# Optimization experiments

Hardware: AMD Instinct MI355X
Metric: run time of the kernel (lower is better)

Reference implementation:

```python
import jax, jax.numpy as jnp
import numpy as np

B, T = 128, 512          # batch, sequence length (padded game length)
F_IN = 19 * 19           # flattened Go board features
H = 128                  # n_hid
P = 19 * 19 + 1          # policy classes: board points + pass


def setup_inputs() -> dict:
    key = jax.random.key(0)
    ks = jax.random.split(key, 8)
    s = 0.05  # init scale
    return {
        "states": jax.random.normal(ks[0], (B, T, F_IN), jnp.float32),
        "moves": jax.random.randint(ks[1], (B, T), 0, P, jnp.int32),
        "values": jax.random.uniform(ks[2], (B, T), jnp.float32, -1.0, 1.0),
        # LSTM layer 0: concat([x, h]) @ W0 + b0, gates [i, f, g, o]
        "W0": jax.random.normal(ks[3], (F_IN + H, 4 * H), jnp.float32) * s,
        "b0": jnp.zeros((4 * H,), jnp.float32),
        # LSTM layer 1
        "W1": jax.random.normal(ks[4], (H + H, 4 * H), jnp.float32) * s,
        "b1": jnp.zeros((4 * H,), jnp.float32),
        # policy head (size**2 + 1 logits), value head (tanh scalar)
        "Wp": jax.random.normal(ks[5], (H, P), jnp.float32) * s,
        "bp": jnp.zeros((P,), jnp.float32),
        "Wv": jax.random.normal(ks[6], (H, 1), jnp.float32) * s,
        "bv": jnp.zeros((1,), jnp.float32),
    }


def _lstm_cell(h, c, x, W, b):
    # TF LSTMCell: z = [x; h] @ W + b, forget bias 1.0
    z = jnp.concatenate([x, h], axis=-1) @ W + b
    i, f, g, o = jnp.split(z, 4, axis=-1)
    c_new = jax.nn.sigmoid(f + 1.0) * c + jax.nn.sigmoid(i) * jnp.tanh(g)
    h_new = jax.nn.sigmoid(o) * jnp.tanh(c_new)
    return h_new, c_new


def reference(states, moves, values, W0, b0, W1, b1, Wp, bp, Wv, bv):
    b = states.shape[0]
    zeros = jnp.zeros((b, H), states.dtype)

    def step(carry, x_t):
        h0, c0, h1, c1 = carry
        h0, c0 = _lstm_cell(h0, c0, x_t, W0, b0)
        h1, c1 = _lstm_cell(h1, c1, h0, W1, b1)
        return (h0, c0, h1, c1), h1

    _, hs = jax.lax.scan(step, (zeros, zeros, zeros, zeros),
                         jnp.swapaxes(states, 0, 1))  # hs: [T, B, H]
    outputs = jnp.swapaxes(hs, 0, 1)                  # [B, T, H]

    policy_logits = outputs @ Wp + bp                 # [B, T, P]
    winners = jnp.tanh(outputs @ Wv + bv)[..., 0]     # [B, T]

    mask = (values != -9.0).astype(jnp.float32)
    n_mask = mask.sum()

    logp = jax.nn.log_softmax(policy_logits, axis=-1)
    xent = -jnp.take_along_axis(logp, moves[..., None].astype(jnp.int32), axis=-1)[..., 0]
    policy_loss = (mask * xent).sum() / n_mask
    value_loss = (mask * jnp.square(winners - values)).sum() / n_mask
    acc = (moves == jnp.argmax(policy_logits, axis=-1).astype(moves.dtype)).astype(jnp.float32).mean()
    return jnp.stack([policy_loss, value_loss, acc])
```

## Files before the change

### kernel.cpp

```cpp
#include <hip/hip_runtime.h>
#include <hip/hip_bf16.h>
#include <stdint.h>


typedef short v8s __attribute__((ext_vector_type(8)));
typedef float v4f __attribute__((ext_vector_type(4)));

#define MFMA_B16(a,b,c) __builtin_amdgcn_mfma_f32_16x16x32_bf16((a),(b),(c),0,0,0)

#define NT     512
#define FIN    361
#define KP0    384
#define NPC    362
#define NPP    368

#define OFF_Z    ((size_t)0)
#define OFF_H0   ((size_t)67108864)
#define OFF_H1   ((size_t)83886080)
#define OFF_W0XT ((size_t)100663296)
#define OFF_WPT  ((size_t)101187584)
#define OFF_B0P  ((size_t)101281792)
#define OFF_BPP  ((size_t)101285888)
#define OFF_ACC  ((size_t)101287936)

static __device__ __forceinline__ short f2b(float f) {
  __hip_bfloat16 h = __float2bfloat16(f);
  union { __hip_bfloat16 h; short s; } cv; cv.h = h; return cv.s;
}
static __device__ __forceinline__ float b2f(unsigned int lo16) {
  union { unsigned u; float f; } cv; cv.u = lo16 << 16; return cv.f;
}

static __device__ __forceinline__ void sync_lds() {
  __builtin_amdgcn_sched_barrier(0);
  asm volatile("s_waitcnt lgkmcnt(0)" ::: "memory");
  __builtin_amdgcn_s_barrier();
  __builtin_amdgcn_sched_barrier(0);
}

__global__ __launch_bounds__(256) void k_conv_weights(
    const float* __restrict__ W0, const float* __restrict__ b0,
    const float* __restrict__ Wp, const float* __restrict__ bp,
    char* __restrict__ ws) {
  int idx = blockIdx.x * 256 + threadIdx.x;
  __hip_bfloat16* W0xT = (__hip_bfloat16*)(ws + OFF_W0XT);
  __hip_bfloat16* WpT  = (__hip_bfloat16*)(ws + OFF_WPT);
  float* b0p = (float*)(ws + OFF_B0P);
  float* bpp = (float*)(ws + OFF_BPP);
  float* acc = (float*)(ws + OFF_ACC);

  if (idx < 196608) {
    int np = idx / 384, k = idx - np * 384;
    int n = (np >> 2) + 128 * (np & 3);
    float v = (k < FIN) ? W0[(size_t)k * 512 + n] : 0.f;
    W0xT[idx] = __float2bfloat16(v);
    return;
  }
  idx -= 196608;
  if (idx < 47104) {
    int p = idx >> 7, k = idx & 127;
    WpT[idx] = __float2bfloat16(p < NPC ? Wp[(size_t)k * NPC + p] : 0.f);
    return;
  }
  idx -= 47104;
  if (idx < 512) {
    int n = (idx >> 2) + 128 * (idx & 3);
    b0p[idx] = b0[n] + (((idx & 3) == 1) ? 1.0f : 0.0f);
    return;
  }
  idx -= 512;
  if (idx < NPP) { bpp[idx] = (idx < NPC) ? bp[idx] : -1e30f; return; }
  idx -= NPP;
  if (idx < 4) { acc[idx] = 0.f; return; }
}

template<int KTOT, bool AF32>
__global__ __launch_bounds__(256) void k_gemm(
    const void* __restrict__ Ap, const __hip_bfloat16* __restrict__ BT,
    const float* __restrict__ bias, __hip_bfloat16* __restrict__ C) {
  __shared__ char sm[65536];
  const int tid = threadIdx.x;
  const int l = tid & 63, wm = tid >> 6;
  const int c = l & 15, lg = l >> 4;
  const int m0 = blockIdx.x * 128;
  const int n0 = blockIdx.y * 128;
  constexpr int NS = KTOT / 64;

  uint4 ra[4], rb[4];
  float fa[32];

  auto LD = [&](int ks) {
#pragma unroll
    for (int i = 0; i < 4; i++) {
      int idx = i * 4096 + tid * 16;
      int row = idx >> 7, colb = idx & 127;
      if constexpr (AF32) {
        int r = m0 + row;
        const float* src = (const float*)Ap + ((size_t)(r & 127) * NT + (r >> 7)) * FIN;
        int kb = ks * 64 + (colb >> 1);
#pragma unroll
        for (int u = 0; u < 8; u++) {
          int kf = kb + u;
          fa[i * 8 + u] = (kf < FIN) ? src[kf] : 0.f;
        }
      } else {
        ra[i] = *(const uint4*)((const char*)Ap + ((size_t)(m0 + row) * KTOT + ks * 64) * 2 + colb);
      }
      rb[i] = *(const uint4*)((const char*)BT + ((size_t)(n0 + row) * KTOT + ks * 64) * 2 + colb);
    }
  };
  auto ST = [&](int bsel) {
#pragma unroll
    for (int i = 0; i < 4; i++) {
      int idx = i * 4096 + tid * 16;
      int row = idx >> 7, colb = idx & 127;
      int sw = colb ^ ((row & 7) << 4);
      if constexpr (AF32) {
        v8s w;
#pragma unroll
        for (int u = 0; u < 8; u++) w[u] = f2b(fa[i * 8 + u]);
        *(v8s*)(sm + bsel * 16384 + row * 128 + sw) = w;
      } else {
        *(uint4*)(sm + bsel * 16384 + row * 128 + sw) = ra[i];
      }
      *(uint4*)(sm + 32768 + bsel * 16384 + row * 128 + sw) = rb[i];
    }
  };

  v4f acc[2][8];
  v4f z4 = {0.f, 0.f, 0.f, 0.f};
#pragma unroll
  for (int mt = 0; mt < 2; mt++)
#pragma unroll
    for (int nt = 0; nt < 8; nt++) acc[mt][nt] = z4;

  LD(0); ST(0);
  __syncthreads();
  for (int ks = 0; ks < NS; ks++) {
    if (ks + 1 < NS) LD(ks + 1);
    const int bsel = ks & 1;
#pragma unroll
    for (int kk = 0; kk < 2; kk++) {
      int bir = kk * 64 + lg * 16;
      v8s af[2];
#pragma unroll
      for (int mt = 0; mt < 2; mt++) {
        int row = wm * 32 + mt * 16 + c;
        af[mt] = *(v8s*)(sm + bsel * 16384 + row * 128 + (bir ^ ((row & 7) << 4)));
      }
#pragma unroll
      for (int nt = 0; nt < 8; nt++) {
        int n = nt * 16 + c;
        v8s bf = *(v8s*)(sm + 32768 + bsel * 16384 + n * 128 + (bir ^ ((n & 7) << 4)));
#pragma unroll
        for (int mt = 0; mt < 2; mt++) acc[mt][nt] = MFMA_B16(af[mt], bf, acc[mt][nt]);
      }
    }
    if (ks + 1 < NS) ST((ks + 1) & 1);
    __syncthreads();
  }

#pragma unroll
  for (int mt = 0; mt < 2; mt++)
#pragma unroll
    for (int nt = 0; nt < 8; nt++) {
      int colp = n0 + nt * 16 + c;
      float bs = bias[colp];
#pragma unroll
      for (int j = 0; j < 4; j++) {
        int row = m0 + wm * 32 + mt * 16 + lg * 4 + j;
        C[(size_t)row * 512 + colp] = __float2bfloat16(acc[mt][nt][j] + bs);
      }
    }
}

__global__ __launch_bounds__(512) void k_scanA(
    const __hip_bfloat16* __restrict__ Z, const float* __restrict__ Wfull,
    int row0, __hip_bfloat16* __restrict__ hout) {
  __shared__ char sm[8192];
  const int tid = threadIdx.x;
  const int l = tid & 63, wv = tid >> 6;
  const int c = l & 15, lg = l >> 4;
  const int b0 = blockIdx.x * 4;
  const int m_ = 16 * wv + c;

  v8s breg[4][4];
#pragma unroll
  for (int g = 0; g < 4; g++) {
    int n = g * 128 + m_;
#pragma unroll
    for (int kk = 0; kk < 4; kk++) {
      v8s w;
#pragma unroll
      for (int i = 0; i < 8; i++)
        w[i] = f2b(Wfull[(size_t)(row0 + kk * 32 + lg * 8 + i) * 512 + n]);
      breg[kk][g] = w;
    }
  }
  for (int e = tid; e < 4096; e += 512) *(short*)(sm + e * 2) = 0;

  float cst = 0.f;
  auto ZLD = [&](int t) -> uint2 {
    return *(const uint2*)(Z + ((size_t)t * 128 + b0 + lg) * 512 + m_ * 4);
  };
  uint2 zA = ZLD(0), zB = ZLD(1), zC;
  __syncthreads();

  v4f z4 = {0.f, 0.f, 0.f, 0.f};
  const int wrow = 4 * lg;
  const int woff = wrow * 256 + ((m_ * 2) ^ ((wrow & 7) << 4));
  for (int t = 0; t < NT; t++) {
    v4f acc[4];
#pragma unroll
    for (int g = 0; g < 4; g++) acc[g] = z4;
    const int hb = (t & 1) * 4096;
#pragma unroll
    for (int kk = 0; kk < 4; kk++) {
      int bir = kk * 64 + lg * 16;
      v8s a = *(v8s*)(sm + hb + c * 256 + (bir ^ ((c & 7) << 4)));
#pragma unroll
      for (int g = 0; g < 4; g++) acc[g] = MFMA_B16(a, breg[kk][g], acc[g]);
    }
    if (t + 2 < NT) zC = ZLD(t + 2);

    float xi = acc[0][0] + b2f(zA.x & 0xffffu);
    float xf = acc[1][0] + b2f(zA.x >> 16);
    float xg = acc[2][0] + b2f(zA.y & 0xffffu);
    float xo = acc[3][0] + b2f(zA.y >> 16);
    float ei = __expf(-xi);
    float ef = __expf(-xf);
    float eg = __expf(2.f * xg);
    float eo = __expf(-xo);
    float cn = cst * __builtin_amdgcn_rcpf(1.f + ef)
             + (eg - 1.f) * __builtin_amdgcn_rcpf((1.f + ei) * (eg + 1.f));
    cst = cn;
    float ec = __expf(2.f * cn);
    float hv = (ec - 1.f) * __builtin_amdgcn_rcpf((1.f + eo) * (ec + 1.f));
    short hbits = f2b(hv);
    *(short*)(sm + ((t + 1) & 1) * 4096 + woff) = hbits;
    union { short s; __hip_bfloat16 h; } cv; cv.s = hbits;
    hout[((size_t)t * 128 + b0 + lg) * 128 + m_] = cv.h;
    zA = zB; zB = zC;
    sync_lds();
  }
}

__global__ __launch_bounds__(512) void k_scanB(
    const unsigned short* __restrict__ H0, const float* __restrict__ W1f,
    const float* __restrict__ b1, __hip_bfloat16* __restrict__ hout) {
  __shared__ char sm[8192];
  const int tid = threadIdx.x;
  const int l = tid & 63, wv = tid >> 6;
  const int c = l & 15, lg = l >> 4;
  const int b0 = blockIdx.x * 4;
  const int m_ = 16 * wv + c;

  v8s bregX[4][4], bregH[4][4];
#pragma unroll
  for (int g = 0; g < 4; g++) {
    int n = g * 128 + m_;
#pragma unroll
    for (int kk = 0; kk < 4; kk++) {
      v8s wx, wh;
#pragma unroll
      for (int i = 0; i < 8; i++) {
        int k = kk * 32 + lg * 8 + i;
        wx[i] = f2b(W1f[(size_t)k * 512 + n]);
        wh[i] = f2b(W1f[(size_t)(128 + k) * 512 + n]);
      }
      bregX[kk][g] = wx; bregH[kk][g] = wh;
    }
  }
  float bq[4];
#pragma unroll
  for (int g = 0; g < 4; g++)
    bq[g] = b1[g * 128 + m_] + ((g == 1) ? 1.0f : 0.0f);
  for (int e = tid; e < 4096; e += 512) *(short*)(sm + e * 2) = 0;

  uint4 u4z = {0u, 0u, 0u, 0u};
  uint4 hqA[4], hqB[4];
#pragma unroll
  for (int kk = 0; kk < 4; kk++) { hqA[kk] = u4z; hqB[kk] = u4z; }
  auto HLD = [&](int t, uint4* dst) {
    if ((c & 3) == 0) {
      const char* p = (const char*)H0 +
          (((size_t)t * 128 + b0 + (c >> 2)) * 128 + lg * 8) * 2;
#pragma unroll
      for (int kk = 0; kk < 4; kk++) dst[kk] = *(const uint4*)(p + kk * 64);
    }
  };
  HLD(0, hqA);

  float cst = 0.f;
  const int wrow = 4 * lg;
  const int woff = wrow * 256 + ((m_ * 2) ^ ((wrow & 7) << 4));
  __syncthreads();

  auto STEP = [&](int t, uint4* cur, uint4* nxt) {
    if (t + 1 < NT) HLD(t + 1, nxt);
    v4f acc[4];
#pragma unroll
    for (int g = 0; g < 4; g++) acc[g] = (v4f){bq[g], bq[g], bq[g], bq[g]};
    const int hb = (t & 1) * 4096;
#pragma unroll
    for (int kk = 0; kk < 4; kk++) {
      int bir = kk * 64 + lg * 16;
      v8s a = *(v8s*)(sm + hb + c * 256 + (bir ^ ((c & 7) << 4)));
#pragma unroll
      for (int g = 0; g < 4; g++) acc[g] = MFMA_B16(a, bregH[kk][g], acc[g]);
    }
#pragma unroll
    for (int kk = 0; kk < 4; kk++) {
      union { uint4 q; v8s v; } u; u.q = cur[kk];
#pragma unroll
      for (int g = 0; g < 4; g++) acc[g] = MFMA_B16(u.v, bregX[kk][g], acc[g]);
    }
    float xi = acc[0][0];
    float xf = acc[1][0];
    float xg = acc[2][0];
    float xo = acc[3][0];
    float ei = __expf(-xi);
    float ef = __expf(-xf);
    float eg = __expf(2.f * xg);
    float eo = __expf(-xo);
    float cn = cst * __builtin_amdgcn_rcpf(1.f + ef)
             + (eg - 1.f) * __builtin_amdgcn_rcpf((1.f + ei) * (eg + 1.f));
    cst = cn;
    float ec = __expf(2.f * cn);
    float hv = (ec - 1.f) * __builtin_amdgcn_rcpf((1.f + eo) * (ec + 1.f));
    short hbits = f2b(hv);
    *(short*)(sm + ((t + 1) & 1) * 4096 + woff) = hbits;
    union { short s; __hip_bfloat16 h; } cv; cv.s = hbits;
    hout[((size_t)t * 128 + b0 + lg) * 128 + m_] = cv.h;
    sync_lds();
  };

  for (int t = 0; t < NT; t += 2) {
    STEP(t, hqA, hqB);
    STEP(t + 1, hqB, hqA);
  }
}

__global__ __launch_bounds__(256) void k_heads(
    const __hip_bfloat16* __restrict__ Hh, const __hip_bfloat16* __restrict__ WpT,
    const float* __restrict__ bpp, const float* __restrict__ Wv,
    const float* __restrict__ bv, const int* __restrict__ moves,
    const float* __restrict__ values, float* __restrict__ accum) {
  __shared__ char sm[110592];
  const int tid = threadIdx.x;
  const int l = tid & 63, wm = tid >> 6;
  const int c = l & 15, lg = l >> 4;
  const int r0 = blockIdx.x * 64;

#pragma unroll
  for (int i = 0; i < 4; i++) {
    int idx = i * 4096 + tid * 16;
    int row = idx >> 8, colb = idx & 255;
    uint4 v = *(const uint4*)((const char*)Hh + (size_t)r0 * 256 + idx);
    *(uint4*)(sm + row * 256 + (colb ^ ((row & 7) << 4))) = v;
  }
#pragma unroll
  for (int i = 0; i < 23; i++) {
    int idx = i * 4096 + tid * 16;
    int row = idx >> 8, colb = idx & 255;
    uint4 v = *(const uint4*)((const char*)WpT + idx);
    *(uint4*)(sm + 16384 + row * 256 + (colb ^ ((row & 7) << 4))) = v;
  }
  __syncthreads();

  v4f acc[23];
  v4f z4 = {0.f, 0.f, 0.f, 0.f};
#pragma unroll
  for (int q = 0; q < 23; q++) acc[q] = z4;
#pragma unroll
  for (int kk = 0; kk < 4; kk++) {
    int bir = kk * 64 + lg * 16;
    int ar = wm * 16 + c;
    v8s a = *(v8s*)(sm + ar * 256 + (bir ^ ((ar & 7) << 4)));
#pragma unroll
    for (int q = 0; q < 23; q++) {
      int n = q * 16 + c;
      v8s b = *(v8s*)(sm + 16384 + n * 256 + (bir ^ ((n & 7) << 4)));
      acc[q] = MFMA_B16(a, b, acc[q]);
    }
  }
  float bq[23];
#pragma unroll
  for (int q = 0; q < 23; q++) bq[q] = bpp[q * 16 + c];

  float tp = 0.f, tv = 0.f, ta = 0.f, tn = 0.f;
#pragma unroll
  for (int j = 0; j < 4; j++) {
    int rloc = lg * 4 + j;
    int r = r0 + wm * 16 + rloc;
    int t = r >> 7, b = r & 127;
    int mv = moves[(size_t)b * NT + t];
    float val = values[(size_t)b * NT + t];
    float msk = (val != -9.0f) ? 1.f : 0.f;

    float pmax = -3.0e38f;
#pragma unroll
    for (int q = 0; q < 23; q++) pmax = fmaxf(pmax, acc[q][j] + bq[q]);
#pragma unroll
    for (int d = 1; d < 16; d <<= 1) pmax = fmaxf(pmax, __shfl_xor(pmax, d, 64));
    float ps = 0.f;
#pragma unroll
    for (int q = 0; q < 23; q++) ps += __expf((acc[q][j] + bq[q]) - pmax);
#pragma unroll
    for (int d = 1; d < 16; d <<= 1) ps += __shfl_xor(ps, d, 64);
    float lse = pmax + __logf(ps);

    int qm = mv >> 4, cm = mv & 15;
    float mlv = 0.f;
#pragma unroll
    for (int q = 0; q < 23; q++) if (q == qm) mlv = acc[q][j] + bq[q];
    mlv = __shfl(mlv, (l & 48) + cm, 64);
    float xent = lse - mlv;

    float amx = -3.0e38f; int aix = 0;
#pragma unroll
    for (int q = 0; q < 23; q++) {
      float v = acc[q][j] + bq[q];
      if (v > amx) { amx = v; aix = q * 16 + c; }
    }
#pragma unroll
    for (int d = 1; d < 16; d <<= 1) {
      float ov = __shfl_xor(amx, d, 64);
      int oi = __shfl_xor(aix, d, 64);
      if (ov > amx || (ov == amx && oi < aix)) { amx = ov; aix = oi; }
    }

    float pd = 0.f;
    int vrow = wm * 16 + rloc;
#pragma unroll
    for (int i = 0; i < 8; i++) {
      int k = c * 8 + i;
      short hv = *(short*)(sm + vrow * 256 + ((k * 2) ^ ((vrow & 7) << 4)));
      pd += b2f((unsigned short)hv) * Wv[k];
    }
#pragma unroll
    for (int d = 1; d < 16; d <<= 1) pd += __shfl_xor(pd, d, 64);
    float eo = __expf(2.f * (pd + bv[0]));
    float win = (eo - 1.f) * __builtin_amdgcn_rcpf(eo + 1.f);
    float dv = win - val;

    if (c == 0) {
      tp += msk * xent;
      tv += msk * dv * dv;
      ta += (aix == mv) ? 1.f : 0.f;
      tn += msk;
    }
  }
  tp += __shfl_xor(tp, 16, 64); tp += __shfl_xor(tp, 32, 64);
  tv += __shfl_xor(tv, 16, 64); tv += __shfl_xor(tv, 32, 64);
  ta += __shfl_xor(ta, 16, 64); ta += __shfl_xor(ta, 32, 64);
  tn += __shfl_xor(tn, 16, 64); tn += __shfl_xor(tn, 32, 64);
  if (l == 0) {
    atomicAdd(accum + 0, tp);
    atomicAdd(accum + 1, tv);
    atomicAdd(accum + 2, ta);
    atomicAdd(accum + 3, tn);
  }
}

__global__ void k_final(const float* __restrict__ accum, float* __restrict__ out) {
  if (threadIdx.x == 0) {
    float nm = accum[3];
    out[0] = accum[0] / nm;
    out[1] = accum[1] / nm;
    out[2] = accum[2] / 65536.0f;
  }
}

extern "C" void kernel_launch(void* const* d_in, const int* in_sizes, int n_in,
                              void* d_out, int out_size, void* d_ws, size_t ws_size,
                              hipStream_t stream) {
  (void)in_sizes; (void)n_in; (void)out_size; (void)ws_size;
  const float* states = (const float*)d_in[0];
  const int*   moves  = (const int*)d_in[1];
  const float* values = (const float*)d_in[2];
  const float* W0 = (const float*)d_in[3];
  const float* b0 = (const float*)d_in[4];
  const float* W1 = (const float*)d_in[5];
  const float* b1 = (const float*)d_in[6];
  const float* Wp = (const float*)d_in[7];
  const float* bp = (const float*)d_in[8];
  const float* Wv = (const float*)d_in[9];
  const float* bv = (const float*)d_in[10];
  char* ws = (char*)d_ws;

  __hip_bfloat16* zbuf = (__hip_bfloat16*)(ws + OFF_Z);
  __hip_bfloat16* h0   = (__hip_bfloat16*)(ws + OFF_H0);
  unsigned short* h0u  = (unsigned short*)(ws + OFF_H0);
  __hip_bfloat16* h1   = (__hip_bfloat16*)(ws + OFF_H1);
  __hip_bfloat16* W0xT = (__hip_bfloat16*)(ws + OFF_W0XT);
  __hip_bfloat16* WpT  = (__hip_bfloat16*)(ws + OFF_WPT);
  float* b0p = (float*)(ws + OFF_B0P);
  float* bpp = (float*)(ws + OFF_BPP);
  float* acc = (float*)(ws + OFF_ACC);

  k_conv_weights<<<956, 256, 0, stream>>>(W0, b0, Wp, bp, ws);
  k_gemm<KP0, true><<<dim3(512, 4), 256, 0, stream>>>(states, W0xT, b0p, zbuf);
  k_scanA<<<32, 512, 0, stream>>>(zbuf, W0, FIN, h0);
  k_scanB<<<32, 512, 0, stream>>>(h0u, W1, b1, h1);
  k_heads<<<1024, 256, 0, stream>>>(h1, WpT, bpp, Wv, bv, moves, values, acc);
  k_final<<<1, 1, 0, stream>>>(acc, (float*)d_out);
}
```

Measured before the change: 1.002 ms.

## Fuse both LSTM layer scans into one wavefront-specialized kernel with FP8 layer-1 MFMA

Result: slower. 1.034 ms (+3.2%).

```diff
diff --git a/kernel.cpp b/kernel.cpp
--- a/kernel.cpp
+++ b/kernel.cpp
@@ -7,6 +7,7 @@
 typedef float v4f __attribute__((ext_vector_type(4)));
 
 #define MFMA_B16(a,b,c) __builtin_amdgcn_mfma_f32_16x16x32_bf16((a),(b),(c),0,0,0)
+#define MFMA_F8(a,b,c)  __builtin_amdgcn_mfma_f32_16x16x32_fp8_fp8((a),(b),(c),0,0,0)
 
 #define NT     512
 #define FIN    361
@@ -15,7 +16,6 @@
 #define NPP    368
 
 #define OFF_Z    ((size_t)0)
-#define OFF_H0   ((size_t)67108864)
 #define OFF_H1   ((size_t)83886080)
 #define OFF_W0XT ((size_t)100663296)
 #define OFF_WPT  ((size_t)101187584)
@@ -29,6 +29,22 @@
 }
 static __device__ __forceinline__ float b2f(unsigned int lo16) {
   union { unsigned u; float f; } cv; cv.u = lo16 << 16; return cv.f;
+}
+static __device__ __forceinline__ unsigned f2e4m3(float f) {
+  union { float f; unsigned u; } cv; cv.f = f;
+  unsigned s = (cv.u >> 31) << 7;
+  float a = fabsf(f);
+  a = fminf(a, 448.f);
+  unsigned code;
+  if (a >= 0.015625f) {
+    union { float f; unsigned u; } m; m.f = a;
+    unsigned u = m.u + 0x7FFFF + ((m.u >> 20) & 1);
+    code = (u >> 20) - 960;
+    if (code > 126u) code = 126u;
+  } else {
+    code = (unsigned)rintf(a * 512.f);
+  }
+  return s | code;
 }
 
 static __device__ __forceinline__ void sync_lds() {
@@ -174,170 +190,140 @@
     }
 }
 
-__global__ __launch_bounds__(512) void k_scanA(
-    const __hip_bfloat16* __restrict__ Z, const float* __restrict__ Wfull,
-    int row0, __hip_bfloat16* __restrict__ hout) {
-  __shared__ char sm[8192];
+__global__ __launch_bounds__(1024, 4) void k_scan12(
+    const __hip_bfloat16* __restrict__ Z, const float* __restrict__ W0f,
+    const float* __restrict__ W1f, const float* __restrict__ b1,
+    __hip_bfloat16* __restrict__ h1out) {
+  __shared__ char sm[16384];
   const int tid = threadIdx.x;
   const int l = tid & 63, wv = tid >> 6;
   const int c = l & 15, lg = l >> 4;
-  const int b0 = blockIdx.x * 4;
-  const int m_ = 16 * wv + c;
-
-  v8s breg[4][4];
-#pragma unroll
-  for (int g = 0; g < 4; g++) {
-    int n = g * 128 + m_;
-#pragma unroll
-    for (int kk = 0; kk < 4; kk++) {
-      v8s w;
-#pragma unroll
-      for (int i = 0; i < 8; i++)
-        w[i] = f2b(Wfull[(size_t)(row0 + kk * 32 + lg * 8 + i) * 512 + n]);
-      breg[kk][g] = w;
-    }
-  }
-  for (int e = tid; e < 4096; e += 512) *(short*)(sm + e * 2) = 0;
-
-  float cst = 0.f;
-  auto ZLD = [&](int t) -> uint2 {
-    return *(const uint2*)(Z + ((size_t)t * 128 + b0 + lg) * 512 + m_ * 4);
-  };
-  uint2 zA = ZLD(0), zB = ZLD(1), zC;
-  __syncthreads();
-
+  const int role = wv >> 3, rw = wv & 7;
+  const int B0 = blockIdx.x * 4;
+  const int m_ = 16 * rw + c;
+  const int row = 4 * lg;
   v4f z4 = {0.f, 0.f, 0.f, 0.f};
-  const int wrow = 4 * lg;
-  const int woff = wrow * 256 + ((m_ * 2) ^ ((wrow & 7) << 4));
-  for (int t = 0; t < NT; t++) {
-    v4f acc[4];
-#pragma unroll
-    for (int g = 0; g < 4; g++) acc[g] = z4;
-    const int hb = (t & 1) * 4096;
-#pragma unroll
-    for (int kk = 0; kk < 4; kk++) {
-      int bir = kk * 64 + lg * 16;
-      v8s a = *(v8s*)(sm + hb + c * 256 + (bir ^ ((c & 7) << 4)));
-#pragma unroll
-      for (int g = 0; g < 4; g++) acc[g] = MFMA_B16(a, breg[kk][g], acc[g]);
-    }
-    if (t + 2 < NT) zC = ZLD(t + 2);
-
-    float xi = acc[0][0] + b2f(zA.x & 0xffffu);
-    float xf = acc[1][0] + b2f(zA.x >> 16);
-    float xg = acc[2][0] + b2f(zA.y & 0xffffu);
-    float xo = acc[3][0] + b2f(zA.y >> 16);
-    float ei = __expf(-xi);
-    float ef = __expf(-xf);
-    float eg = __expf(2.f * xg);
-    float eo = __expf(-xo);
-    float cn = cst * __builtin_amdgcn_rcpf(1.f + ef)
-             + (eg - 1.f) * __builtin_amdgcn_rcpf((1.f + ei) * (eg + 1.f));
-    cst = cn;
-    float ec = __expf(2.f * cn);
-    float hv = (ec - 1.f) * __builtin_amdgcn_rcpf((1.f + eo) * (ec + 1.f));
-    short hbits = f2b(hv);
-    *(short*)(sm + ((t + 1) & 1) * 4096 + woff) = hbits;
-    union { short s; __hip_bfloat16 h; } cv; cv.s = hbits;
-    hout[((size_t)t * 128 + b0 + lg) * 128 + m_] = cv.h;
-    zA = zB; zB = zC;
+
+  for (int e = tid * 4; e < 16384; e += 1024 * 4) *(int*)(sm + e) = 0;
+
+  if (role == 0) {
+    v8s breg[4][4];
+#pragma unroll
+    for (int kk = 0; kk < 4; kk++)
+#pragma unroll
+      for (int g = 0; g < 4; g++) {
+        int n = g * 128 + m_;
+        v8s w;
+#pragma unroll
+        for (int i = 0; i < 8; i++)
+          w[i] = f2b(W0f[(size_t)(FIN + kk * 32 + lg * 8 + i) * 512 + n]);
+        breg[kk][g] = w;
+      }
+
+    uint2 zA, zB, zC;
+    auto ZLD = [&](int t) -> uint2 {
+      return *(const uint2*)(Z + ((size_t)t * 128 + B0 + lg) * 512 + m_ * 4);
+    };
+    zA = ZLD(0); zB = ZLD(1);
+    float cst = 0.f;
+    const int wb16 = row * 256 + (((m_ >> 3) ^ row) << 4) + ((m_ * 2) & 15);
+    const int wf8  = row * 128 + (((m_ >> 3) ^ row) << 3) + (m_ & 7);
+    __syncthreads();
+
+    for (int s = 0; s < NT; s++) {
+      const int abase = ((s + 1) & 1) * 4096;
+      v4f acc[4];
+#pragma unroll
+      for (int g = 0; g < 4; g++) acc[g] = z4;
+#pragma unroll
+      for (int kk = 0; kk < 4; kk++) {
+        v8s a = *(v8s*)(sm + abase + c * 256 + ((((kk * 4 + lg) ^ c) & 15) << 4));
+#pragma unroll
+        for (int g = 0; g < 4; g++) acc[g] = MFMA_B16(a, breg[kk][g], acc[g]);
+      }
+      if (s + 2 < NT) zC = ZLD(s + 2);
+
+      float xi = acc[0][0] + b2f(zA.x & 0xffffu);
+      float xf = acc[1][0] + b2f(zA.x >> 16);
+      float xg = acc[2][0] + b2f(zA.y & 0xffffu);
+      float xo = acc[3][0] + b2f(zA.y >> 16);
+      float ei = __expf(-xi);
+      float ef = __expf(-xf);
+      float eg = __expf(2.f * xg);
+      float eo = __expf(-xo);
+      float cn = cst * __builtin_amdgcn_rcpf(1.f + ef)
+               + (eg - 1.f) * __builtin_amdgcn_rcpf((1.f + ei) * (eg + 1.f));
+      cst = cn;
+      float ec = __expf(2.f * cn);
+      float hv = (ec - 1.f) * __builtin_amdgcn_rcpf((1.f + eo) * (ec + 1.f));
+      *(short*)(sm + (s & 1) * 4096 + wb16) = f2b(hv);
+      *(unsigned char*)(sm + 8192 + (s & 1) * 2048 + wf8) = (unsigned char)f2e4m3(hv);
+      zA = zB; zB = zC;
+      sync_lds();
+    }
     sync_lds();
-  }
-}
-
-__global__ __launch_bounds__(512) void k_scanB(
-    const unsigned short* __restrict__ H0, const float* __restrict__ W1f,
-    const float* __restrict__ b1, __hip_bfloat16* __restrict__ hout) {
-  __shared__ char sm[8192];
-  const int tid = threadIdx.x;
-  const int l = tid & 63, wv = tid >> 6;
-  const int c = l & 15, lg = l >> 4;
-  const int b0 = blockIdx.x * 4;
-  const int m_ = 16 * wv + c;
-
-  v8s bregX[4][4], bregH[4][4];
-#pragma unroll
-  for (int g = 0; g < 4; g++) {
-    int n = g * 128 + m_;
-#pragma unroll
-    for (int kk = 0; kk < 4; kk++) {
-      v8s wx, wh;
-#pragma unroll
-      for (int i = 0; i < 8; i++) {
-        int k = kk * 32 + lg * 8 + i;
-        wx[i] = f2b(W1f[(size_t)k * 512 + n]);
-        wh[i] = f2b(W1f[(size_t)(128 + k) * 512 + n]);
-      }
-      bregX[kk][g] = wx; bregH[kk][g] = wh;
-    }
-  }
-  float bq[4];
-#pragma unroll
-  for (int g = 0; g < 4; g++)
-    bq[g] = b1[g * 128 + m_] + ((g == 1) ? 1.0f : 0.0f);
-  for (int e = tid; e < 4096; e += 512) *(short*)(sm + e * 2) = 0;
-
-  uint4 u4z = {0u, 0u, 0u, 0u};
-  uint4 hqA[4], hqB[4];
-#pragma unroll
-  for (int kk = 0; kk < 4; kk++) { hqA[kk] = u4z; hqB[kk] = u4z; }
-  auto HLD = [&](int t, uint4* dst) {
-    if ((c & 3) == 0) {
-      const char* p = (const char*)H0 +
-          (((size_t)t * 128 + b0 + (c >> 2)) * 128 + lg * 8) * 2;
-#pragma unroll
-      for (int kk = 0; kk < 4; kk++) dst[kk] = *(const uint4*)(p + kk * 64);
-    }
-  };
-  HLD(0, hqA);
-
-  float cst = 0.f;
-  const int wrow = 4 * lg;
-  const int woff = wrow * 256 + ((m_ * 2) ^ ((wrow & 7) << 4));
-  __syncthreads();
-
-  auto STEP = [&](int t, uint4* cur, uint4* nxt) {
-    if (t + 1 < NT) HLD(t + 1, nxt);
-    v4f acc[4];
-#pragma unroll
-    for (int g = 0; g < 4; g++) acc[g] = (v4f){bq[g], bq[g], bq[g], bq[g]};
-    const int hb = (t & 1) * 4096;
-#pragma unroll
-    for (int kk = 0; kk < 4; kk++) {
-      int bir = kk * 64 + lg * 16;
-      v8s a = *(v8s*)(sm + hb + c * 256 + (bir ^ ((c & 7) << 4)));
-#pragma unroll
-      for (int g = 0; g < 4; g++) acc[g] = MFMA_B16(a, bregH[kk][g], acc[g]);
-    }
-#pragma unroll
-    for (int kk = 0; kk < 4; kk++) {
-      union { uint4 q; v8s v; } u; u.q = cur[kk];
-#pragma unroll
-      for (int g = 0; g < 4; g++) acc[g] = MFMA_B16(u.v, bregX[kk][g], acc[g]);
-    }
-    float xi = acc[0][0];
-    float xf = acc[1][0];
-    float xg = acc[2][0];
-    float xo = acc[3][0];
-    float ei = __expf(-xi);
-    float ef = __expf(-xf);
-    float eg = __expf(2.f * xg);
-    float eo = __expf(-xo);
-    float cn = cst * __builtin_amdgcn_rcpf(1.f + ef)
-             + (eg - 1.f) * __builtin_amdgcn_rcpf((1.f + ei) * (eg + 1.f));
-    cst = cn;
-    float ec = __expf(2.f * cn);
-    float hv = (ec - 1.f) * __builtin_amdgcn_rcpf((1.f + eo) * (ec + 1.f));
-    short hbits = f2b(hv);
-    *(short*)(sm + ((t + 1) & 1) * 4096 + woff) = hbits;
-    union { short s; __hip_bfloat16 h; } cv; cv.s = hbits;
-    hout[((size_t)t * 128 + b0 + lg) * 128 + m_] = cv.h;
+  } else {
+    unsigned long long bregH[4][4], bregX[4][4];
+#pragma unroll
+    for (int kk = 0; kk < 4; kk++)
+#pragma unroll
+      for (int g = 0; g < 4; g++) {
+        int n = g * 128 + m_;
+        unsigned long long wh = 0ull, wx = 0ull;
+#pragma unroll
+        for (int i = 0; i < 8; i++) {
+          int k = kk * 32 + lg * 8 + i;
+          wh |= (unsigned long long)f2e4m3(W1f[(size_t)(128 + k) * 512 + n]) << (8 * i);
+          wx |= (unsigned long long)f2e4m3(W1f[(size_t)k * 512 + n]) << (8 * i);
+        }
+        bregH[kk][g] = wh;
+        bregX[kk][g] = wx;
+      }
+    float bq[4];
+#pragma unroll
+    for (int g = 0; g < 4; g++)
+      bq[g] = b1[g * 128 + m_] + ((g == 1) ? 1.0f : 0.0f);
+    float cst = 0.f;
+    const int wf8 = row * 128 + (((m_ >> 3) ^ row) << 3) + (m_ & 7);
+    __syncthreads();
     sync_lds();
-  };
-
-  for (int t = 0; t < NT; t += 2) {
-    STEP(t, hqA, hqB);
-    STEP(t + 1, hqB, hqA);
+
+    for (int s = 1; s <= NT; s++) {
+      const int hbase = 12288 + (s & 1) * 2048;
+      const int xbase = 8192 + ((s + 1) & 1) * 2048;
+      v4f acc[4];
+#pragma unroll
+      for (int g = 0; g < 4; g++) acc[g] = (v4f){bq[g], bq[g], bq[g], bq[g]};
+#pragma unroll
+      for (int kk = 0; kk < 4; kk++) {
+        long ah = *(const long*)(sm + hbase + c * 128 + ((((kk * 4 + lg) ^ c) & 15) << 3));
+#pragma unroll
+        for (int g = 0; g < 4; g++) acc[g] = MFMA_F8(ah, (long)bregH[kk][g], acc[g]);
+      }
+#pragma unroll
+      for (int kk = 0; kk < 4; kk++) {
+        long ax = *(const long*)(sm + xbase + c * 128 + ((((kk * 4 + lg) ^ c) & 15) << 3));
+#pragma unroll
+        for (int g = 0; g < 4; g++) acc[g] = MFMA_F8(ax, (long)bregX[kk][g], acc[g]);
+      }
+
+      float xi = acc[0][0], xf = acc[1][0], xg = acc[2][0], xo = acc[3][0];
+      float ei = __expf(-xi);
+      float ef = __expf(-xf);
+      float eg = __expf(2.f * xg);
+      float eo = __expf(-xo);
+      float cn = cst * __builtin_amdgcn_rcpf(1.f + ef)
+               + (eg - 1.f) * __builtin_amdgcn_rcpf((1.f + ei) * (eg + 1.f));
+      cst = cn;
+      float ec = __expf(2.f * cn);
+      float hv = (ec - 1.f) * __builtin_amdgcn_rcpf((1.f + eo) * (ec + 1.f));
+      short hbits = f2b(hv);
+      *(unsigned char*)(sm + 12288 + ((s + 1) & 1) * 2048 + wf8) =
+          (unsigned char)f2e4m3(hv);
+      union { short s; __hip_bfloat16 h; } cv; cv.s = hbits;
+      h1out[((size_t)(s - 1) * 128 + B0 + lg) * 128 + m_] = cv.h;
+      sync_lds();
+    }
   }
 }
 
@@ -490,8 +476,6 @@
   char* ws = (char*)d_ws;
 
   __hip_bfloat16* zbuf = (__hip_bfloat16*)(ws + OFF_Z);
-  __hip_bfloat16* h0   = (__hip_bfloat16*)(ws + OFF_H0);
-  unsigned short* h0u  = (unsigned short*)(ws + OFF_H0);
   __hip_bfloat16* h1   = (__hip_bfloat16*)(ws + OFF_H1);
   __hip_bfloat16* W0xT = (__hip_bfloat16*)(ws + OFF_W0XT);
   __hip_bfloat16* WpT  = (__hip_bfloat16*)(ws + OFF_WPT);
@@ -501,8 +485,7 @@
 
   k_conv_weights<<<956, 256, 0, stream>>>(W0, b0, Wp, bp, ws);
   k_gemm<KP0, true><<<dim3(512, 4), 256, 0, stream>>>(states, W0xT, b0p, zbuf);
-  k_scanA<<<32, 512, 0, stream>>>(zbuf, W0, FIN, h0);
-  k_scanB<<<32, 512, 0, stream>>>(h0u, W1, b1, h1);
+  k_scan12<<<32, 1024, 0, stream>>>(zbuf, W0, W1, b1, h1);
   k_heads<<<1024, 256, 0, stream>>>(h1, WpT, bpp, Wv, bv, moves, values, acc);
   k_final<<<1, 1, 0, stream>>>(acc, (float*)d_out);
 }
```
